# Optimization experiments

Measured on AMD Instinct MI355X. Metric: run time of the kernel, lower is better.

Reference implementation:

```python
import jax, jax.numpy as jnp
import numpy as np

N_S, N_T, E = 50000, 50000, 600000
D_IN, D_H, D_OUT = 256, 128, 64


def setup_inputs() -> dict:
    key = jax.random.key(0)
    k1, k2, k3, k4, k5, k6 = jax.random.split(key, 6)
    edge_src = jax.random.randint(k1, (E,), 0, N_S, dtype=jnp.int32)
    edge_dst = jax.random.randint(k2, (E,), 0, N_T, dtype=jnp.int32)
    edge_index = jnp.stack([edge_src, edge_dst], axis=0)  # [2, E]
    x_s = jax.random.normal(k3, (N_S, D_IN), dtype=jnp.float32)
    x_t = jax.random.normal(k4, (N_T, D_IN), dtype=jnp.float32)
    W0 = jax.random.normal(k5, (D_IN, D_H), dtype=jnp.float32) * (1.0 / np.sqrt(D_IN))
    W1 = jax.random.normal(k6, (D_H, D_OUT), dtype=jnp.float32) * (1.0 / np.sqrt(D_H))
    return {"edge_index": edge_index, "x_s": x_s, "x_t": x_t, "W0": W0, "W1": W1}


def gcn_conv(x, src, dst, W):
    """PyG GCNConv, bias=False: D^{-1/2}(A+I)D^{-1/2} (x @ W)."""
    N = x.shape[0]
    h = x @ W  # [N, out]
    loops = jnp.arange(N, dtype=src.dtype)
    s = jnp.concatenate([src, loops])  # add self-loops
    d = jnp.concatenate([dst, loops])
    deg = jax.ops.segment_sum(jnp.ones_like(d, dtype=h.dtype), d, num_segments=N)
    dinv = jnp.where(deg > 0, jax.lax.rsqrt(deg), 0.0)
    norm = dinv[s] * dinv[d]  # [E+N]
    return jax.ops.segment_sum(h[s] * norm[:, None], d, num_segments=N)


def reference(edge_index, x_s, x_t, W0, W1):
    n_s = x_s.shape[0]
    src = edge_index[0]
    dst = edge_index[1] + n_s  # targets live in the x_t block
    acts = [jax.nn.relu, lambda v: v]
    Ws = [W0, W1]
    for W, act in zip(Ws, acts):
        x = jnp.concatenate([x_s, x_t], axis=0)
        x = act(gcn_conv(x, src, dst, W))
        x_s, x_t = x[:n_s], x[n_s:]
    return (x_s, x_t)
```

## Files before the change

### kernel.cpp

```cpp
#include <hip/hip_runtime.h>
#include <cstdint>
#include <cstddef>

typedef unsigned short u16;
typedef unsigned int   u32;
typedef __attribute__((ext_vector_type(8))) short bf16x8;
typedef __attribute__((ext_vector_type(4))) float f32x4;

#define D_IN  256
#define D_H   128
#define D_OUT 64
#define LSTR  72

__device__ __forceinline__ float bf2f(u16 u){
  union { u32 i; float f; } v; v.i = ((u32)u) << 16; return v.f;
}
__device__ __forceinline__ u16 f2bf(float f){
  union { float f; u32 i; } v; v.f = f;
  u32 r = (v.i + 0x7fffu + ((v.i >> 16) & 1u)) >> 16;
  return (u16)r;
}

__global__ void k_wprep(const float* __restrict__ W0, const float* __restrict__ W1,
                        u16* __restrict__ W0t, u16* __restrict__ W1t,
                        int* __restrict__ deg, int n_t){
  int i = blockIdx.x * 256 + threadIdx.x;
  if (i < 128 * 256){
    int n = i >> 8, k = i & 255;
    W0t[i] = f2bf(W0[(size_t)k * 128 + n]);
  } else if (i < 128 * 256 + 64 * 128){
    int j = i - 128 * 256;
    int n = j >> 7, k = j & 127;
    W1t[j] = f2bf(W1[(size_t)k * 64 + n]);
  } else if (i - (128 * 256 + 64 * 128) < n_t){
    deg[i - (128 * 256 + 64 * 128)] = 0;
  }
}

__global__ void k_deg(const int* __restrict__ dst, int E, int* __restrict__ deg){
  int e = blockIdx.x * 256 + threadIdx.x;
  if (e < E) atomicAdd(&deg[dst[e]], 1);
}

__global__ __launch_bounds__(256) void k_bsum(const int* __restrict__ deg, int N,
                                              int* __restrict__ bsum){
  __shared__ int s[256];
  int tid = threadIdx.x;
  int i = blockIdx.x * 256 + tid;
  s[tid] = (i < N) ? deg[i] : 0;
  __syncthreads();
  for (int o = 128; o > 0; o >>= 1){
    if (tid < o) s[tid] += s[tid + o];
    __syncthreads();
  }
  if (tid == 0) bsum[blockIdx.x] = s[0];
}

__global__ __launch_bounds__(256) void k_bscan(int* __restrict__ bsum, int nb){
  __shared__ int s[256];
  int tid = threadIdx.x;
  int v = (tid < nb) ? bsum[tid] : 0;
  s[tid] = v;
  __syncthreads();
  for (int o = 1; o < 256; o <<= 1){
    int t = (tid >= o) ? s[tid - o] : 0;
    __syncthreads();
    s[tid] += t;
    __syncthreads();
  }
  if (tid < nb) bsum[tid] = s[tid] - v;
}

__global__ __launch_bounds__(256) void k_off(const int* __restrict__ deg, int N,
                                             const int* __restrict__ bsum,
                                             int* __restrict__ off, int* __restrict__ cursor,
                                             float* __restrict__ dinv){
  __shared__ int s[256];
  int tid = threadIdx.x;
  int i = blockIdx.x * 256 + tid;
  int v = (i < N) ? deg[i] : 0;
  s[tid] = v;
  __syncthreads();
  for (int o = 1; o < 256; o <<= 1){
    int t = (tid >= o) ? s[tid - o] : 0;
    __syncthreads();
    s[tid] += t;
    __syncthreads();
  }
  if (i < N){
    int excl = s[tid] - v + bsum[blockIdx.x];
    off[i] = excl;
    cursor[i] = excl;
    dinv[i] = rsqrtf((float)v + 1.0f);
  }
}

__global__ void k_fill(const int* __restrict__ src, const int* __restrict__ dst,
                       int E, int* __restrict__ cursor, int* __restrict__ csr){
  int e = blockIdx.x * 256 + threadIdx.x;
  if (e < E){
    int d = dst[e];
    int p = atomicAdd(&cursor[d], 1);
    csr[p] = src[e];
  }
}

__global__ __launch_bounds__(256) void k_gemm1(
    const float* __restrict__ Xs, const float* __restrict__ Xt,
    const u16* __restrict__ W0t, int M, int n_s,
    u16* __restrict__ out)
{
  __shared__ u16 As[128 * LSTR];
  __shared__ u16 Bs[128 * LSTR];
  const int t    = threadIdx.x;
  const int wave = t >> 6, lane = t & 63;
  const int wm   = (wave >> 1) * 64, wn = (wave & 1) * 64;
  const int lm   = lane & 15, quad = lane >> 4;
  const int row0 = blockIdx.x * 128;

  f32x4 acc[4][4];
  const f32x4 z = {0.f, 0.f, 0.f, 0.f};
  #pragma unroll
  for (int i = 0; i < 4; i++)
    #pragma unroll
    for (int j = 0; j < 4; j++) acc[i][j] = z;

  const int ar = t >> 1;
  const int kh = (t & 1) * 32;
  const int r  = row0 + ar;
  const float* xp = nullptr;
  if (r < M) xp = (r < n_s) ? (Xs + (size_t)r * D_IN) : (Xt + (size_t)(r - n_s) * D_IN);
  const u16* wrow = W0t + (size_t)ar * D_IN + kh;

  float4 a4[8];
  int4   b4[4];
  if (xp){
    #pragma unroll
    for (int j = 0; j < 8; j++) a4[j] = *(const float4*)(xp + kh + j * 4);
  } else {
    float4 zz = make_float4(0,0,0,0);
    #pragma unroll
    for (int j = 0; j < 8; j++) a4[j] = zz;
  }
  #pragma unroll
  for (int j = 0; j < 4; j++) b4[j] = *(const int4*)(wrow + j * 8);

  for (int k0 = 0; k0 < D_IN; k0 += 64){
    __syncthreads();
    {
      u16 abuf[32];
      #pragma unroll
      for (int j = 0; j < 8; j++){
        abuf[j*4+0] = f2bf(a4[j].x); abuf[j*4+1] = f2bf(a4[j].y);
        abuf[j*4+2] = f2bf(a4[j].z); abuf[j*4+3] = f2bf(a4[j].w);
      }
      u16* ap = &As[ar * LSTR + kh];
      *(int4*)(ap +  0) = *(int4*)&abuf[0];
      *(int4*)(ap +  8) = *(int4*)&abuf[8];
      *(int4*)(ap + 16) = *(int4*)&abuf[16];
      *(int4*)(ap + 24) = *(int4*)&abuf[24];
      u16* bp = &Bs[ar * LSTR + kh];
      *(int4*)(bp +  0) = b4[0];
      *(int4*)(bp +  8) = b4[1];
      *(int4*)(bp + 16) = b4[2];
      *(int4*)(bp + 24) = b4[3];
    }
    __syncthreads();

    if (k0 + 64 < D_IN){
      if (xp){
        #pragma unroll
        for (int j = 0; j < 8; j++) a4[j] = *(const float4*)(xp + k0 + 64 + kh + j * 4);
      }
      #pragma unroll
      for (int j = 0; j < 4; j++) b4[j] = *(const int4*)(wrow + k0 + 64 + j * 8);
    }

    #pragma unroll
    for (int kk = 0; kk < 64; kk += 32){
      bf16x8 af[4], bfr[4];
      #pragma unroll
      for (int i = 0; i < 4; i++)
        af[i] = *(const bf16x8*)&As[(wm + i*16 + lm) * LSTR + kk + quad*8];
      #pragma unroll
      for (int i = 0; i < 4; i++)
        bfr[i] = *(const bf16x8*)&Bs[(wn + i*16 + lm) * LSTR + kk + quad*8];
      #pragma unroll
      for (int mi = 0; mi < 4; mi++)
        #pragma unroll
        for (int ni = 0; ni < 4; ni++)
          acc[mi][ni] = __builtin_amdgcn_mfma_f32_16x16x32_bf16(
              af[mi], bfr[ni], acc[mi][ni], 0, 0, 0);
    }
  }

  #pragma unroll
  for (int mi = 0; mi < 4; mi++){
    int rbase = row0 + wm + mi * 16 + quad * 4;
    #pragma unroll
    for (int rr = 0; rr < 4; rr++){
      int m = rbase + rr;
      if (m >= M) continue;
      u16* op = out + (size_t)m * D_H + wn + lm;
      #pragma unroll
      for (int ni = 0; ni < 4; ni++)
        op[ni * 16] = f2bf(acc[mi][ni][rr]);
    }
  }
}

__global__ __launch_bounds__(256) void k_aggf(
    const int* __restrict__ off, const int* __restrict__ deg,
    const int* __restrict__ csr, const float* __restrict__ dinv,
    u16* __restrict__ h1, int n_s, int n_t)
{
  int w    = (blockIdx.x * 256 + threadIdx.x) >> 6;
  int lane = threadIdx.x & 63;
  if (w >= n_t) return;
  int start = off[w];
  int n     = deg[w];

  float r0 = 0.f, r1 = 0.f, p0 = 0.f, p1 = 0.f;
  int i = 0;
  for (; i + 4 <= n; i += 4){
    int sa = csr[start + i];
    int sb = csr[start + i + 1];
    int sc = csr[start + i + 2];
    int sd = csr[start + i + 3];
    u32 da = *(const u32*)(h1 + (size_t)sa * D_H + lane * 2);
    u32 db = *(const u32*)(h1 + (size_t)sb * D_H + lane * 2);
    u32 dc = *(const u32*)(h1 + (size_t)sc * D_H + lane * 2);
    u32 dd = *(const u32*)(h1 + (size_t)sd * D_H + lane * 2);
    float va0 = bf2f((u16)da), va1 = bf2f((u16)(da >> 16));
    float vb0 = bf2f((u16)db), vb1 = bf2f((u16)(db >> 16));
    float vc0 = bf2f((u16)dc), vc1 = bf2f((u16)(dc >> 16));
    float vd0 = bf2f((u16)dd), vd1 = bf2f((u16)(dd >> 16));
    r0 += va0 + vb0 + vc0 + vd0;
    r1 += va1 + vb1 + vc1 + vd1;
    p0 += fmaxf(va0,0.f) + fmaxf(vb0,0.f) + fmaxf(vc0,0.f) + fmaxf(vd0,0.f);
    p1 += fmaxf(va1,0.f) + fmaxf(vb1,0.f) + fmaxf(vc1,0.f) + fmaxf(vd1,0.f);
  }
  for (; i < n; i++){
    int sa = csr[start + i];
    u32 da = *(const u32*)(h1 + (size_t)sa * D_H + lane * 2);
    float va0 = bf2f((u16)da), va1 = bf2f((u16)(da >> 16));
    r0 += va0; r1 += va1;
    p0 += fmaxf(va0,0.f); p1 += fmaxf(va1,0.f);
  }

  float di  = dinv[w];
  float di2 = di * di;
  u32* selfp = (u32*)(h1 + (size_t)(n_s + w) * D_H + lane * 2);
  u32 ht = *selfp;
  float z0 = fmaxf(di * r0 + di2 * bf2f((u16)ht), 0.f);
  float z1 = fmaxf(di * r1 + di2 * bf2f((u16)(ht >> 16)), 0.f);
  float u0 = di * p0 + di2 * z0;
  float u1 = di * p1 + di2 * z1;
  *selfp = (u32)f2bf(u0) | ((u32)f2bf(u1) << 16);
}

__global__ __launch_bounds__(256) void k_gemm2(
    const u16* __restrict__ h1, const u16* __restrict__ W1t,
    int M, int n_s, float* __restrict__ out)
{
  __shared__ u16 As[128 * LSTR];
  __shared__ u16 Bs[64 * LSTR];
  const int t    = threadIdx.x;
  const int wave = t >> 6, lane = t & 63;
  const int wm   = wave * 32;
  const int lm   = lane & 15, quad = lane >> 4;
  const int row0 = blockIdx.x * 128;

  f32x4 acc[2][4];
  const f32x4 z = {0.f, 0.f, 0.f, 0.f};
  #pragma unroll
  for (int i = 0; i < 2; i++)
    #pragma unroll
    for (int j = 0; j < 4; j++) acc[i][j] = z;

  const int ar = t >> 1;
  const int kh = (t & 1) * 32;
  const int r  = row0 + ar;
  const bool relu_a = (r < n_s);
  const int bn = t >> 2;
  const int bk = (t & 3) * 16;

  int4 a4[4], w4[2];
  if (r < M){
    const u16* hp = h1 + (size_t)r * D_H + kh;
    #pragma unroll
    for (int j = 0; j < 4; j++) a4[j] = *(const int4*)(hp + j * 8);
  } else {
    int4 zz = make_int4(0,0,0,0);
    #pragma unroll
    for (int j = 0; j < 4; j++) a4[j] = zz;
  }
  w4[0] = *(const int4*)(W1t + (size_t)bn * D_H + bk);
  w4[1] = *(const int4*)(W1t + (size_t)bn * D_H + bk + 8);

  for (int k0 = 0; k0 < D_H; k0 += 64){
    __syncthreads();
    {
      u16 abuf[32];
      #pragma unroll
      for (int j = 0; j < 4; j++){
        u16* hh = (u16*)&a4[j];
        #pragma unroll
        for (int q = 0; q < 8; q++){
          u16 v = hh[q];
          abuf[j*8+q] = (relu_a && (v & 0x8000u)) ? (u16)0 : v;
        }
      }
      u16* ap = &As[ar * LSTR + kh];
      *(int4*)(ap +  0) = *(int4*)&abuf[0];
      *(int4*)(ap +  8) = *(int4*)&abuf[8];
      *(int4*)(ap + 16) = *(int4*)&abuf[16];
      *(int4*)(ap + 24) = *(int4*)&abuf[24];
      u16* bp = &Bs[bn * LSTR + bk];
      *(int4*)(bp + 0) = w4[0];
      *(int4*)(bp + 8) = w4[1];
    }
    __syncthreads();

    if (k0 + 64 < D_H){
      if (r < M){
        const u16* hp = h1 + (size_t)r * D_H + k0 + 64 + kh;
        #pragma unroll
        for (int j = 0; j < 4; j++) a4[j] = *(const int4*)(hp + j * 8);
      }
      w4[0] = *(const int4*)(W1t + (size_t)bn * D_H + k0 + 64 + bk);
      w4[1] = *(const int4*)(W1t + (size_t)bn * D_H + k0 + 64 + bk + 8);
    }

    #pragma unroll
    for (int kk = 0; kk < 64; kk += 32){
      bf16x8 af[2], bfr[4];
      #pragma unroll
      for (int i = 0; i < 2; i++)
        af[i] = *(const bf16x8*)&As[(wm + i*16 + lm) * LSTR + kk + quad*8];
      #pragma unroll
      for (int i = 0; i < 4; i++)
        bfr[i] = *(const bf16x8*)&Bs[(i*16 + lm) * LSTR + kk + quad*8];
      #pragma unroll
      for (int mi = 0; mi < 2; mi++)
        #pragma unroll
        for (int ni = 0; ni < 4; ni++)
          acc[mi][ni] = __builtin_amdgcn_mfma_f32_16x16x32_bf16(
              af[mi], bfr[ni], acc[mi][ni], 0, 0, 0);
    }
  }

  #pragma unroll
  for (int mi = 0; mi < 2; mi++){
    int rbase = row0 + wm + mi * 16 + quad * 4;
    #pragma unroll
    for (int rr = 0; rr < 4; rr++){
      int m = rbase + rr;
      if (m >= M) continue;
      float* op = out + (size_t)m * D_OUT + lm;
      #pragma unroll
      for (int ni = 0; ni < 4; ni++)
        op[ni * 16] = acc[mi][ni][rr];
    }
  }
}

static inline size_t alup(size_t x){ return (x + 255) & ~(size_t)255; }

extern "C" void kernel_launch(void* const* d_in, const int* in_sizes, int n_in,
                              void* d_out, int out_size, void* d_ws, size_t ws_size,
                              hipStream_t stream)
{
  const int*   ei = (const int*)d_in[0];
  const float* xs = (const float*)d_in[1];
  const float* xt = (const float*)d_in[2];
  const float* W0 = (const float*)d_in[3];
  const float* W1 = (const float*)d_in[4];
  const int E   = in_sizes[0] / 2;
  const int n_s = in_sizes[1] / D_IN;
  const int n_t = in_sizes[2] / D_IN;
  const int M   = n_s + n_t;
  const int* src = ei;
  const int* dst = ei + E;
  const int nb_t = (n_t + 255) / 256;

  char* p = (char*)d_ws;
  int*   deg    = (int*)p;    p += alup((size_t)n_t * 4);
  int*   off    = (int*)p;    p += alup((size_t)n_t * 4);
  int*   cursor = (int*)p;    p += alup((size_t)n_t * 4);
  float* dinv   = (float*)p;  p += alup((size_t)n_t * 4);
  int*   bsum   = (int*)p;    p += alup((size_t)nb_t * 4);
  int*   csr    = (int*)p;    p += alup((size_t)E * 4);
  u16*   W0t    = (u16*)p;    p += alup((size_t)D_H * D_IN * 2);
  u16*   W1t    = (u16*)p;    p += alup((size_t)D_OUT * D_H * 2);
  u16*   h1     = (u16*)p;    p += alup((size_t)M * D_H * 2);

  const int wprep_n = 128*256 + 64*128 + n_t;
  k_wprep <<<(wprep_n + 255) / 256, 256, 0, stream>>>(W0, W1, W0t, W1t, deg, n_t);
  k_deg   <<<(E + 255) / 256, 256, 0, stream>>>(dst, E, deg);
  k_bsum  <<<nb_t, 256, 0, stream>>>(deg, n_t, bsum);
  k_bscan <<<1, 256, 0, stream>>>(bsum, nb_t);
  k_off   <<<nb_t, 256, 0, stream>>>(deg, n_t, bsum, off, cursor, dinv);
  k_fill  <<<(E + 255) / 256, 256, 0, stream>>>(src, dst, E, cursor, csr);

  k_gemm1<<<(M + 127) / 128, 256, 0, stream>>>(xs, xt, W0t, M, n_s, h1);
  k_aggf <<<(n_t + 3) / 4, 256, 0, stream>>>(off, deg, csr, dinv, h1, n_s, n_t);
  k_gemm2<<<(M + 127) / 128, 256, 0, stream>>>(h1, W1t, M, n_s, (float*)d_out);
}
```

Measured before the change: 285.0 us.

## Halve GEMM row tiles and vectorize aggregation gathers with 16-byte per-lane loads

Both GEMM kernels move from 128-row to 64-row tiles, which doubles the block count so M=100000 rows spread across more CUs, and it shrinks per-thread register and LDS use. The aggregation kernel now splits each wave into four groups of 16 lanes. Each group gathers a different neighbor row with 16-byte loads, and the groups combine their partial sums with cross-lane shuffles before one group writes the result. The aim is fewer, wider memory transactions on the random gathers. In exchange, the GEMM loses some B-tile reuse per block, and the aggregation pays extra shuffles and partial-group work when a node's degree is not a multiple of four.

```diff
diff --git a/kernel.cpp b/kernel.cpp
--- a/kernel.cpp
+++ b/kernel.cpp
@@ -110,37 +110,39 @@
     const u16* __restrict__ W0t, int M, int n_s,
     u16* __restrict__ out)
 {
-  __shared__ u16 As[128 * LSTR];
+  __shared__ u16 As[64 * LSTR];
   __shared__ u16 Bs[128 * LSTR];
   const int t    = threadIdx.x;
   const int wave = t >> 6, lane = t & 63;
-  const int wm   = (wave >> 1) * 64, wn = (wave & 1) * 64;
+  const int wm   = (wave >> 1) * 32, wn = (wave & 1) * 64;
   const int lm   = lane & 15, quad = lane >> 4;
-  const int row0 = blockIdx.x * 128;
-
-  f32x4 acc[4][4];
+  const int row0 = blockIdx.x * 64;
+
+  f32x4 acc[2][4];
   const f32x4 z = {0.f, 0.f, 0.f, 0.f};
   #pragma unroll
-  for (int i = 0; i < 4; i++)
+  for (int i = 0; i < 2; i++)
     #pragma unroll
     for (int j = 0; j < 4; j++) acc[i][j] = z;
 
-  const int ar = t >> 1;
-  const int kh = (t & 1) * 32;
+  const int ar = t >> 2;
+  const int kq = (t & 3) * 16;
   const int r  = row0 + ar;
   const float* xp = nullptr;
   if (r < M) xp = (r < n_s) ? (Xs + (size_t)r * D_IN) : (Xt + (size_t)(r - n_s) * D_IN);
-  const u16* wrow = W0t + (size_t)ar * D_IN + kh;
-
-  float4 a4[8];
+  const int bn = t >> 1;
+  const int bk = (t & 1) * 32;
+  const u16* wrow = W0t + (size_t)bn * D_IN + bk;
+
+  float4 a4[4];
   int4   b4[4];
   if (xp){
     #pragma unroll
-    for (int j = 0; j < 8; j++) a4[j] = *(const float4*)(xp + kh + j * 4);
+    for (int j = 0; j < 4; j++) a4[j] = *(const float4*)(xp + kq + j * 4);
   } else {
     float4 zz = make_float4(0,0,0,0);
     #pragma unroll
-    for (int j = 0; j < 8; j++) a4[j] = zz;
+    for (int j = 0; j < 4; j++) a4[j] = zz;
   }
   #pragma unroll
   for (int j = 0; j < 4; j++) b4[j] = *(const int4*)(wrow + j * 8);
@@ -148,18 +150,16 @@
   for (int k0 = 0; k0 < D_IN; k0 += 64){
     __syncthreads();
     {
-      u16 abuf[32];
-      #pragma unroll
-      for (int j = 0; j < 8; j++){
+      u16 abuf[16];
+      #pragma unroll
+      for (int j = 0; j < 4; j++){
         abuf[j*4+0] = f2bf(a4[j].x); abuf[j*4+1] = f2bf(a4[j].y);
         abuf[j*4+2] = f2bf(a4[j].z); abuf[j*4+3] = f2bf(a4[j].w);
       }
-      u16* ap = &As[ar * LSTR + kh];
-      *(int4*)(ap +  0) = *(int4*)&abuf[0];
-      *(int4*)(ap +  8) = *(int4*)&abuf[8];
-      *(int4*)(ap + 16) = *(int4*)&abuf[16];
-      *(int4*)(ap + 24) = *(int4*)&abuf[24];
-      u16* bp = &Bs[ar * LSTR + kh];
+      u16* ap = &As[ar * LSTR + kq];
+      *(int4*)(ap + 0) = *(int4*)&abuf[0];
+      *(int4*)(ap + 8) = *(int4*)&abuf[8];
+      u16* bp = &Bs[bn * LSTR + bk];
       *(int4*)(bp +  0) = b4[0];
       *(int4*)(bp +  8) = b4[1];
       *(int4*)(bp + 16) = b4[2];
@@ -170,7 +170,7 @@
     if (k0 + 64 < D_IN){
       if (xp){
         #pragma unroll
-        for (int j = 0; j < 8; j++) a4[j] = *(const float4*)(xp + k0 + 64 + kh + j * 4);
+        for (int j = 0; j < 4; j++) a4[j] = *(const float4*)(xp + k0 + 64 + kq + j * 4);
       }
       #pragma unroll
       for (int j = 0; j < 4; j++) b4[j] = *(const int4*)(wrow + k0 + 64 + j * 8);
@@ -178,15 +178,15 @@
 
     #pragma unroll
     for (int kk = 0; kk < 64; kk += 32){
-      bf16x8 af[4], bfr[4];
-      #pragma unroll
-      for (int i = 0; i < 4; i++)
+      bf16x8 af[2], bfr[4];
+      #pragma unroll
+      for (int i = 0; i < 2; i++)
         af[i] = *(const bf16x8*)&As[(wm + i*16 + lm) * LSTR + kk + quad*8];
       #pragma unroll
       for (int i = 0; i < 4; i++)
         bfr[i] = *(const bf16x8*)&Bs[(wn + i*16 + lm) * LSTR + kk + quad*8];
       #pragma unroll
-      for (int mi = 0; mi < 4; mi++)
+      for (int mi = 0; mi < 2; mi++)
         #pragma unroll
         for (int ni = 0; ni < 4; ni++)
           acc[mi][ni] = __builtin_amdgcn_mfma_f32_16x16x32_bf16(
@@ -195,7 +195,7 @@
   }
 
   #pragma unroll
-  for (int mi = 0; mi < 4; mi++){
+  for (int mi = 0; mi < 2; mi++){
     int rbase = row0 + wm + mi * 16 + quad * 4;
     #pragma unroll
     for (int rr = 0; rr < 4; rr++){
@@ -217,83 +217,100 @@
   int w    = (blockIdx.x * 256 + threadIdx.x) >> 6;
   int lane = threadIdx.x & 63;
   if (w >= n_t) return;
+  const int g = lane >> 4;
+  const int c = lane & 15;
   int start = off[w];
   int n     = deg[w];
 
-  float r0 = 0.f, r1 = 0.f, p0 = 0.f, p1 = 0.f;
+  float r[8], p[8];
+  #pragma unroll
+  for (int q = 0; q < 8; q++){ r[q] = 0.f; p[q] = 0.f; }
+
   int i = 0;
-  for (; i + 4 <= n; i += 4){
-    int sa = csr[start + i];
-    int sb = csr[start + i + 1];
-    int sc = csr[start + i + 2];
-    int sd = csr[start + i + 3];
-    u32 da = *(const u32*)(h1 + (size_t)sa * D_H + lane * 2);
-    u32 db = *(const u32*)(h1 + (size_t)sb * D_H + lane * 2);
-    u32 dc = *(const u32*)(h1 + (size_t)sc * D_H + lane * 2);
-    u32 dd = *(const u32*)(h1 + (size_t)sd * D_H + lane * 2);
-    float va0 = bf2f((u16)da), va1 = bf2f((u16)(da >> 16));
-    float vb0 = bf2f((u16)db), vb1 = bf2f((u16)(db >> 16));
-    float vc0 = bf2f((u16)dc), vc1 = bf2f((u16)(dc >> 16));
-    float vd0 = bf2f((u16)dd), vd1 = bf2f((u16)(dd >> 16));
-    r0 += va0 + vb0 + vc0 + vd0;
-    r1 += va1 + vb1 + vc1 + vd1;
-    p0 += fmaxf(va0,0.f) + fmaxf(vb0,0.f) + fmaxf(vc0,0.f) + fmaxf(vd0,0.f);
-    p1 += fmaxf(va1,0.f) + fmaxf(vb1,0.f) + fmaxf(vc1,0.f) + fmaxf(vd1,0.f);
-  }
-  for (; i < n; i++){
-    int sa = csr[start + i];
-    u32 da = *(const u32*)(h1 + (size_t)sa * D_H + lane * 2);
-    float va0 = bf2f((u16)da), va1 = bf2f((u16)(da >> 16));
-    r0 += va0; r1 += va1;
-    p0 += fmaxf(va0,0.f); p1 += fmaxf(va1,0.f);
-  }
-
-  float di  = dinv[w];
-  float di2 = di * di;
-  u32* selfp = (u32*)(h1 + (size_t)(n_s + w) * D_H + lane * 2);
-  u32 ht = *selfp;
-  float z0 = fmaxf(di * r0 + di2 * bf2f((u16)ht), 0.f);
-  float z1 = fmaxf(di * r1 + di2 * bf2f((u16)(ht >> 16)), 0.f);
-  float u0 = di * p0 + di2 * z0;
-  float u1 = di * p1 + di2 * z1;
-  *selfp = (u32)f2bf(u0) | ((u32)f2bf(u1) << 16);
+  for (; i + 8 <= n; i += 8){
+    int sa = csr[start + i + g];
+    int sb = csr[start + i + 4 + g];
+    int4 da = *(const int4*)(h1 + (size_t)sa * D_H + c * 8);
+    int4 db = *(const int4*)(h1 + (size_t)sb * D_H + c * 8);
+    const u16* ha = (const u16*)&da;
+    const u16* hb = (const u16*)&db;
+    #pragma unroll
+    for (int q = 0; q < 8; q++){
+      float va = bf2f(ha[q]), vb = bf2f(hb[q]);
+      r[q] += va + vb;
+      p[q] += fmaxf(va, 0.f) + fmaxf(vb, 0.f);
+    }
+  }
+  for (; i < n; i += 4){
+    if (i + g < n){
+      int sa = csr[start + i + g];
+      int4 da = *(const int4*)(h1 + (size_t)sa * D_H + c * 8);
+      const u16* ha = (const u16*)&da;
+      #pragma unroll
+      for (int q = 0; q < 8; q++){
+        float va = bf2f(ha[q]);
+        r[q] += va;
+        p[q] += fmaxf(va, 0.f);
+      }
+    }
+  }
+
+  #pragma unroll
+  for (int q = 0; q < 8; q++){
+    r[q] += __shfl_xor(r[q], 16, 64);
+    r[q] += __shfl_xor(r[q], 32, 64);
+    p[q] += __shfl_xor(p[q], 16, 64);
+    p[q] += __shfl_xor(p[q], 32, 64);
+  }
+
+  if (g == 0){
+    float di  = dinv[w];
+    float di2 = di * di;
+    u16* selfp = h1 + (size_t)(n_s + w) * D_H + c * 8;
+    int4 hs = *(const int4*)selfp;
+    const u16* hh = (const u16*)&hs;
+    u16 ob[8];
+    #pragma unroll
+    for (int q = 0; q < 8; q++){
+      float zq = fmaxf(di * r[q] + di2 * bf2f(hh[q]), 0.f);
+      float uq = di * p[q] + di2 * zq;
+      ob[q] = f2bf(uq);
+    }
+    *(int4*)selfp = *(int4*)ob;
+  }
 }
 
 __global__ __launch_bounds__(256) void k_gemm2(
     const u16* __restrict__ h1, const u16* __restrict__ W1t,
     int M, int n_s, float* __restrict__ out)
 {
-  __shared__ u16 As[128 * LSTR];
+  __shared__ u16 As[64 * LSTR];
   __shared__ u16 Bs[64 * LSTR];
   const int t    = threadIdx.x;
   const int wave = t >> 6, lane = t & 63;
-  const int wm   = wave * 32;
+  const int wm   = wave * 16;
   const int lm   = lane & 15, quad = lane >> 4;
-  const int row0 = blockIdx.x * 128;
-
-  f32x4 acc[2][4];
+  const int row0 = blockIdx.x * 64;
+
+  f32x4 acc[4];
   const f32x4 z = {0.f, 0.f, 0.f, 0.f};
   #pragma unroll
-  for (int i = 0; i < 2; i++)
-    #pragma unroll
-    for (int j = 0; j < 4; j++) acc[i][j] = z;
-
-  const int ar = t >> 1;
-  const int kh = (t & 1) * 32;
+  for (int j = 0; j < 4; j++) acc[j] = z;
+
+  const int ar = t >> 2;
+  const int kq = (t & 3) * 16;
   const int r  = row0 + ar;
   const bool relu_a = (r < n_s);
   const int bn = t >> 2;
   const int bk = (t & 3) * 16;
 
-  int4 a4[4], w4[2];
+  int4 a4[2], w4[2];
   if (r < M){
-    const u16* hp = h1 + (size_t)r * D_H + kh;
-    #pragma unroll
-    for (int j = 0; j < 4; j++) a4[j] = *(const int4*)(hp + j * 8);
+    const u16* hp = h1 + (size_t)r * D_H + kq;
+    a4[0] = *(const int4*)(hp);
+    a4[1] = *(const int4*)(hp + 8);
   } else {
-    int4 zz = make_int4(0,0,0,0);
-    #pragma unroll
-    for (int j = 0; j < 4; j++) a4[j] = zz;
+    a4[0] = make_int4(0,0,0,0); a4[1] = a4[0];
   }
   w4[0] = *(const int4*)(W1t + (size_t)bn * D_H + bk);
   w4[1] = *(const int4*)(W1t + (size_t)bn * D_H + bk + 8);
@@ -301,9 +318,9 @@
   for (int k0 = 0; k0 < D_H; k0 += 64){
     __syncthreads();
     {
-      u16 abuf[32];
-      #pragma unroll
-      for (int j = 0; j < 4; j++){
+      u16 abuf[16];
+      #pragma unroll
+      for (int j = 0; j < 2; j++){
         u16* hh = (u16*)&a4[j];
         #pragma unroll
         for (int q = 0; q < 8; q++){
@@ -311,11 +328,9 @@
           abuf[j*8+q] = (relu_a && (v & 0x8000u)) ? (u16)0 : v;
         }
       }
-      u16* ap = &As[ar * LSTR + kh];
-      *(int4*)(ap +  0) = *(int4*)&abuf[0];
-      *(int4*)(ap +  8) = *(int4*)&abuf[8];
-      *(int4*)(ap + 16) = *(int4*)&abuf[16];
-      *(int4*)(ap + 24) = *(int4*)&abuf[24];
+      u16* ap = &As[ar * LSTR + kq];
+      *(int4*)(ap + 0) = *(int4*)&abuf[0];
+      *(int4*)(ap + 8) = *(int4*)&abuf[8];
       u16* bp = &Bs[bn * LSTR + bk];
       *(int4*)(bp + 0) = w4[0];
       *(int4*)(bp + 8) = w4[1];
@@ -324,9 +339,9 @@
 
     if (k0 + 64 < D_H){
       if (r < M){
-        const u16* hp = h1 + (size_t)r * D_H + k0 + 64 + kh;
-        #pragma unroll
-        for (int j = 0; j < 4; j++) a4[j] = *(const int4*)(hp + j * 8);
+        const u16* hp = h1 + (size_t)r * D_H + k0 + 64 + kq;
+        a4[0] = *(const int4*)(hp);
+        a4[1] = *(const int4*)(hp + 8);
       }
       w4[0] = *(const int4*)(W1t + (size_t)bn * D_H + k0 + 64 + bk);
       w4[1] = *(const int4*)(W1t + (size_t)bn * D_H + k0 + 64 + bk + 8);
@@ -334,25 +349,21 @@
 
     #pragma unroll
     for (int kk = 0; kk < 64; kk += 32){
-      bf16x8 af[2], bfr[4];
-      #pragma unroll
-      for (int i = 0; i < 2; i++)
-        af[i] = *(const bf16x8*)&As[(wm + i*16 + lm) * LSTR + kk + quad*8];
+      bf16x8 af;
+      bf16x8 bfr[4];
+      af = *(const bf16x8*)&As[(wm + lm) * LSTR + kk + quad*8];
       #pragma unroll
       for (int i = 0; i < 4; i++)
         bfr[i] = *(const bf16x8*)&Bs[(i*16 + lm) * LSTR + kk + quad*8];
       #pragma unroll
-      for (int mi = 0; mi < 2; mi++)
-        #pragma unroll
-        for (int ni = 0; ni < 4; ni++)
-          acc[mi][ni] = __builtin_amdgcn_mfma_f32_16x16x32_bf16(
-              af[mi], bfr[ni], acc[mi][ni], 0, 0, 0);
-    }
-  }
-
-  #pragma unroll
-  for (int mi = 0; mi < 2; mi++){
-    int rbase = row0 + wm + mi * 16 + quad * 4;
+      for (int ni = 0; ni < 4; ni++)
+        acc[ni] = __builtin_amdgcn_mfma_f32_16x16x32_bf16(
+            af, bfr[ni], acc[ni], 0, 0, 0);
+    }
+  }
+
+  {
+    int rbase = row0 + wm + quad * 4;
     #pragma unroll
     for (int rr = 0; rr < 4; rr++){
       int m = rbase + rr;
@@ -360,7 +371,7 @@
       float* op = out + (size_t)m * D_OUT + lm;
       #pragma unroll
       for (int ni = 0; ni < 4; ni++)
-        op[ni * 16] = acc[mi][ni][rr];
+        op[ni * 16] = acc[ni][rr];
     }
   }
 }
@@ -403,7 +414,7 @@
   k_off   <<<nb_t, 256, 0, stream>>>(deg, n_t, bsum, off, cursor, dinv);
   k_fill  <<<(E + 255) / 256, 256, 0, stream>>>(src, dst, E, cursor, csr);
 
-  k_gemm1<<<(M + 127) / 128, 256, 0, stream>>>(xs, xt, W0t, M, n_s, h1);
+  k_gemm1<<<(M + 63) / 64, 256, 0, stream>>>(xs, xt, W0t, M, n_s, h1);
   k_aggf <<<(n_t + 3) / 4, 256, 0, stream>>>(off, deg, csr, dinv, h1, n_s, n_t);
-  k_gemm2<<<(M + 127) / 128, 256, 0, stream>>>(h1, W1t, M, n_s, (float*)d_out);
-}
+  k_gemm2<<<(M + 63) / 64, 256, 0, stream>>>(h1, W1t, M, n_s, (float*)d_out);
+}
```

Result: slower. 292.1 us (+2.5%).
